# Kernel tuning notes

Measured on AMD Instinct MI355X. Metric: run time of the kernel, lower is better.

The kernel has to match this reference:

```python
import jax, jax.numpy as jnp
import numpy as np
import math

B, T, C, H = 2, 2048, 1024, 16


def setup_inputs() -> dict:
    key = jax.random.key(0)
    k1, k2, k3 = jax.random.split(key, 3)
    x = jax.random.normal(k1, (B, T, C), dtype=jnp.float32)
    qkv_w = jax.random.normal(k2, (3 * C, C), dtype=jnp.float32) * 0.02
    proj_w = jax.random.normal(k3, (C, C), dtype=jnp.float32) * 0.02
    distance_scales = jnp.full((H,), 0.1, dtype=jnp.float32)
    return {"x": x, "qkv_w": qkv_w, "proj_w": proj_w, "distance_scales": distance_scales}


def reference(x, qkv_w, proj_w, distance_scales):
    b, t, c = x.shape
    h = distance_scales.shape[0]
    dh = c // h
    scale = 1.0 / math.sqrt(dh)

    # torch Linear: y = x @ W^T ; split into q, k, v
    qkv = jnp.einsum('btc,oc->bto', x, qkv_w)  # [B,T,3C]
    q, k, v = jnp.split(qkv, 3, axis=-1)
    q = q.reshape(b, t, h, dh).transpose(0, 2, 1, 3)  # [B,H,T,Dh]
    k = k.reshape(b, t, h, dh).transpose(0, 2, 1, 3)
    v = v.reshape(b, t, h, dh).transpose(0, 2, 1, 3)

    logits = jnp.einsum('bhid,bhjd->bhij', q, k) * scale  # [B,H,T,T]

    idx = jnp.arange(t)
    dists = jnp.abs(idx[:, None] - idx[None, :]).astype(x.dtype)  # [T,T]
    logits = logits - distance_scales[None, :, None, None] * dists

    causal = idx[None, :] > idx[:, None]  # True above diagonal -> masked
    logits = jnp.where(causal[None, None, :, :], -jnp.inf, logits)

    attn = jax.nn.softmax(logits, axis=-1)  # [B,H,T,T]

    dist_energy = (attn * dists).sum(axis=-1).mean()
    flop_energy = -(attn * jnp.log(attn + 1e-9)).sum(axis=-1).mean()

    out = jnp.einsum('bhij,bhjd->bhid', attn, v)  # [B,H,T,Dh]
    out = out.transpose(0, 2, 1, 3).reshape(b, t, c)
    out = jnp.einsum('btc,oc->bto', out, proj_w)

    return (out, dist_energy, flop_energy, jax.lax.stop_gradient(attn), jax.lax.stop_gradient(dists))
```

## Files before the change

kernel.cpp:

```cpp
#include <hip/hip_runtime.h>
#include <hip/hip_bf16.h>
#include <math.h>

#define T_SEQ 2048
#define C3 3072
#define C_DIM 1024

typedef __bf16 bf16_t;
typedef __bf16 bf16x8 __attribute__((ext_vector_type(8)));
typedef __bf16 bf16x4_t __attribute__((ext_vector_type(4)));
typedef float f32x4 __attribute__((ext_vector_type(4)));

typedef __attribute__((address_space(1))) const void gconst_t;
typedef __attribute__((address_space(3))) void lds_t;

static __device__ __forceinline__ bf16x8 ldg8(const bf16_t* p) {
    return *reinterpret_cast<const bf16x8*>(p);
}

__global__ __launch_bounds__(256) void aux_kernel(const float* __restrict__ x,
                                                  const float* __restrict__ qw,
                                                  const float* __restrict__ pw,
                                                  bf16_t* __restrict__ xb,
                                                  bf16_t* __restrict__ wb,
                                                  bf16_t* __restrict__ pb,
                                                  float* __restrict__ dout,
                                                  float* __restrict__ ews) {
    long gid = (long)blockIdx.x * 256 + threadIdx.x;
    if (gid < 2) ews[gid] = 0.f;
    const float* src;
    bf16_t* dst;
    long u;
    if (gid < 1048576) { src = x; dst = xb; u = gid; }
    else if (gid < 1835008) { src = qw; dst = wb; u = gid - 1048576; }
    else if (gid < 2097152) { src = pw; dst = pb; u = gid - 1835008; }
    else {
        long v = gid - 2097152;
        long e0 = v << 2;
        int i = (int)(e0 >> 11), j0 = (int)(e0 & 2047);
        f32x4 o;
        for (int r = 0; r < 4; ++r) {
            int j = j0 + r;
            o[r] = (float)(i > j ? i - j : j - i);
        }
        __builtin_nontemporal_store(o, (f32x4*)(dout + e0));
        return;
    }
    float4 v4 = ((const float4*)src)[u];
    bf16x4_t o;
    o[0] = (bf16_t)v4.x; o[1] = (bf16_t)v4.y; o[2] = (bf16_t)v4.z; o[3] = (bf16_t)v4.w;
    *(bf16x4_t*)(dst + u * 4) = o;
}

template <int BM, bool OUT_BF16>
__global__ __launch_bounds__(256) void gemm_bt(const bf16_t* __restrict__ A,
                                               const bf16_t* __restrict__ Bw,
                                               void* __restrict__ Cout,
                                               int M, int N, int K) {
    constexpr int WM = BM / 2;
    constexpr int MI = WM / 16;
    __shared__ bf16_t sA[BM * 64];
    __shared__ bf16_t sB[128 * 64];
    int tid = threadIdx.x, lane = tid & 63, wid = tid >> 6;
    int m = lane & 15, quad = lane >> 4;
    int wm = (wid >> 1) * WM, wn = (wid & 1) * 64;
    int m0 = blockIdx.y * BM, n0 = blockIdx.x * 128;
    int lrow = lane >> 3, cxor = (lane & 7) ^ (lrow & 7);

    const bf16_t* Ag = A + (size_t)(m0 + wid * 8 + lrow) * K + cxor * 8;
    const bf16_t* Bg = Bw + (size_t)(n0 + wid * 8 + lrow) * K + cxor * 8;

    f32x4 acc[MI][4] = {};
    for (int k0 = 0; k0 < K; k0 += 64) {
        for (int p = 0; p < BM / 32; ++p)
            __builtin_amdgcn_global_load_lds((gconst_t*)(Ag + (size_t)(p * 32) * K + k0),
                                             (lds_t*)(sA + (p * 32 + wid * 8) * 64), 16, 0, 0);
        for (int p = 0; p < 4; ++p)
            __builtin_amdgcn_global_load_lds((gconst_t*)(Bg + (size_t)(p * 32) * K + k0),
                                             (lds_t*)(sB + (p * 32 + wid * 8) * 64), 16, 0, 0);
        __syncthreads();
        for (int ks = 0; ks < 2; ++ks) {
            bf16x8 a[MI], b[4];
            for (int i = 0; i < MI; ++i) {
                int r = wm + i * 16 + m;
                a[i] = *(const bf16x8*)(sA + r * 64 + ((((ks << 2) + quad) ^ (r & 7)) << 3));
            }
            for (int j = 0; j < 4; ++j) {
                int r = wn + j * 16 + m;
                b[j] = *(const bf16x8*)(sB + r * 64 + ((((ks << 2) + quad) ^ (r & 7)) << 3));
            }
            for (int i = 0; i < MI; ++i)
                for (int j = 0; j < 4; ++j)
                    acc[i][j] = __builtin_amdgcn_mfma_f32_16x16x32_bf16(b[j], a[i], acc[i][j], 0, 0, 0);
        }
        __syncthreads();
    }
    for (int i = 0; i < MI; ++i)
        for (int j = 0; j < 4; ++j) {
            size_t row = m0 + wm + i * 16 + m;
            int col = n0 + wn + j * 16 + quad * 4;
            if (OUT_BF16) {
                bf16x4_t o;
                for (int r = 0; r < 4; ++r) o[r] = (bf16_t)acc[i][j][r];
                *(bf16x4_t*)((bf16_t*)Cout + row * N + col) = o;
            } else {
                *(f32x4*)((float*)Cout + row * N + col) = acc[i][j];
            }
        }
}

__global__ __launch_bounds__(256) void repack_vt(const bf16_t* __restrict__ qkv,
                                                 bf16_t* __restrict__ vt) {
    __shared__ bf16_t s[64][72];
    int t0 = (blockIdx.x & 31) << 6;
    int bh = blockIdx.x >> 5;
    int b = bh >> 4, h = bh & 15;
    int tid = threadIdx.x;
    int r = tid >> 3, c8 = (tid & 7) << 3;
    const bf16_t* src = qkv + (size_t)(b * T_SEQ) * C3 + 2048 + h * 64;
    for (int p = 0; p < 2; ++p) {
        int t = r + p * 32;
        *(uint4*)&s[t][c8] = *(const uint4*)&src[(size_t)(t0 + t) * C3 + c8];
    }
    __syncthreads();
    bf16_t* dst = vt + (size_t)bh * 64 * T_SEQ;
    for (int p = 0; p < 2; ++p) {
        int d = r + p * 32;
        bf16x8 vv;
        for (int i = 0; i < 8; ++i) vv[i] = s[c8 + i][d];
        *(bf16x8*)&dst[(size_t)d * T_SEQ + t0 + c8] = vv;
    }
}

__global__ __launch_bounds__(256) void attn_kernel(const bf16_t* __restrict__ qkv,
                                                   const bf16_t* __restrict__ vt,
                                                   const float* __restrict__ dscales,
                                                   float* __restrict__ attn,
                                                   bf16_t* __restrict__ y,
                                                   float* __restrict__ ews) {
    __shared__ bf16_t sP[64][72];
    __shared__ float sred[8];
    int base = blockIdx.x & 31;
    int bh = blockIdx.x >> 5;
    int it = (bh & 8) ? (31 - base) : base;
    int b = bh >> 4, h = bh & 15;
    int i0 = it << 6;
    int tid = threadIdx.x, lane = tid & 63, wid = tid >> 6;
    int m = lane & 15, quad = lane >> 4;
    int w16 = wid << 4;
    float dsc = dscales[h];
    const float scale = 0.125f;

    int jskip = 0;
    if (dsc > 1e-6f) {
        int keep = (int)(38.0f / dsc + 63.0f) >> 6;
        jskip = it - keep;
        if (jskip < 0) jskip = 0;
    }

    const bf16_t* Qb = qkv + (size_t)(b * T_SEQ) * C3 + h * 64;
    const bf16_t* Kb = Qb + 1024;
    const bf16_t* Vb = vt + (size_t)bh * 64 * T_SEQ;
    float* Ab = attn + ((size_t)bh * T_SEQ + i0) * T_SEQ;

    int i = i0 + w16 + m;
    bf16x8 qf[2];
    qf[0] = ldg8(Qb + (size_t)i * C3 + quad * 8);
    qf[1] = ldg8(Qb + (size_t)i * C3 + 32 + quad * 8);

    float lsum = 0.f;
    for (int jt = jskip; jt <= it; ++jt) {
        int j0 = jt << 6;
        f32x4 acc[4] = {};
        for (int ks = 0; ks < 2; ++ks)
            for (int n = 0; n < 4; ++n) {
                bf16x8 kf = ldg8(Kb + (size_t)(j0 + n * 16 + m) * C3 + ks * 32 + quad * 8);
                acc[n] = __builtin_amdgcn_mfma_f32_16x16x32_bf16(kf, qf[ks], acc[n], 0, 0, 0);
            }
        if (jt < it) {
            for (int n = 0; n < 4; ++n)
                for (int r = 0; r < 4; ++r) {
                    float d = (float)(i - (j0 + n * 16 + quad * 4 + r));
                    lsum += __expf(acc[n][r] * scale - dsc * d);
                }
        } else {
            for (int n = 0; n < 4; ++n)
                for (int r = 0; r < 4; ++r) {
                    int j = j0 + n * 16 + quad * 4 + r;
                    if (j <= i) lsum += __expf(acc[n][r] * scale - dsc * (float)(i - j));
                }
        }
    }
    lsum += __shfl_xor(lsum, 16);
    lsum += __shfl_xor(lsum, 32);
    float rl = 1.f / lsum;

    f32x4 oacc[4] = {};
    float e_d = 0.f;
    float e_e = (quad == 0) ? -__logf(lsum) : 0.f;

    for (int jt = jskip; jt <= it; ++jt) {
        int j0 = jt << 6;
        f32x4 acc[4] = {};
        for (int ks = 0; ks < 2; ++ks)
            for (int n = 0; n < 4; ++n) {
                bf16x8 kf = ldg8(Kb + (size_t)(j0 + n * 16 + m) * C3 + ks * 32 + quad * 8);
                acc[n] = __builtin_amdgcn_mfma_f32_16x16x32_bf16(kf, qf[ks], acc[n], 0, 0, 0);
            }
        bool diag = (jt == it);
        for (int n = 0; n < 4; ++n) {
            f32x4 pv;
            for (int r = 0; r < 4; ++r) {
                int j = j0 + n * 16 + quad * 4 + r;
                float p = 0.f;
                if (!diag || j <= i) {
                    float d = (float)(i - j);
                    float v = acc[n][r] * scale - dsc * d;
                    p = __expf(v) * rl;
                    e_d += p * d;
                    e_e += p * v;
                }
                pv[r] = p;
            }
            __builtin_nontemporal_store(
                pv, (f32x4*)(Ab + (size_t)(w16 + m) * T_SEQ + j0 + n * 16 + quad * 4));
            bf16x4_t pb;
            for (int r = 0; r < 4; ++r) pb[r] = (bf16_t)pv[r];
            *(bf16x4_t*)&sP[w16 + m][n * 16 + quad * 4] = pb;
        }
        for (int ks = 0; ks < 2; ++ks) {
            bf16x8 pf = *(const bf16x8*)&sP[w16 + m][ks * 32 + quad * 8];
            for (int n = 0; n < 4; ++n) {
                bf16x8 vf = ldg8(Vb + (size_t)(n * 16 + m) * T_SEQ + j0 + ks * 32 + quad * 8);
                oacc[n] = __builtin_amdgcn_mfma_f32_16x16x32_bf16(vf, pf, oacc[n], 0, 0, 0);
            }
        }
    }

    for (int n = 0; n < 4; ++n) {
        bf16x4_t o;
        for (int r = 0; r < 4; ++r) o[r] = (bf16_t)oacc[n][r];
        *(bf16x4_t*)(y + (size_t)(b * T_SEQ + i) * C_DIM + h * 64 + n * 16 + quad * 4) = o;
    }

    for (int off = 1; off < 64; off <<= 1) {
        e_d += __shfl_xor(e_d, off);
        e_e += __shfl_xor(e_e, off);
    }
    if (lane == 0) { sred[wid] = e_d; sred[wid + 4] = e_e; }
    __syncthreads();
    if (tid == 0) {
        atomicAdd(ews, sred[0] + sred[1] + sred[2] + sred[3]);
        atomicAdd(ews + 1, sred[4] + sred[5] + sred[6] + sred[7]);
    }

    {
        f32x4 z4 = {0.f, 0.f, 0.f, 0.f};
        int ln = jskip << 6;
        for (int r = 0; r < 64; ++r) {
            float* rowp = Ab + (size_t)r * T_SEQ;
            for (int c = tid << 2; c < ln; c += 1024)
                __builtin_nontemporal_store(z4, (f32x4*)(rowp + c));
        }
        int zc0 = i0 + 64, zn = T_SEQ - zc0;
        for (int r = 0; r < 64; ++r) {
            float* rowp = Ab + (size_t)r * T_SEQ + zc0;
            for (int c = tid << 2; c < zn; c += 1024)
                __builtin_nontemporal_store(z4, (f32x4*)(rowp + c));
        }
    }
}

__global__ void finalize_kernel(const float* __restrict__ ews, float* __restrict__ dout) {
    dout[4194304] = ews[0] / 65536.f;
    dout[4194305] = -ews[1] / 65536.f;
}

extern "C" void kernel_launch(void* const* d_in, const int* in_sizes, int n_in,
                              void* d_out, int out_size, void* d_ws, size_t ws_size,
                              hipStream_t stream) {
    const float* x = (const float*)d_in[0];
    const float* qkv_w = (const float*)d_in[1];
    const float* proj_w = (const float*)d_in[2];
    const float* dscales = (const float*)d_in[3];
    float* out = (float*)d_out;

    char* ws = (char*)d_ws;
    float* ews   = (float*)ws;
    bf16_t* xb   = (bf16_t*)(ws + 256);
    bf16_t* wb   = xb + 4194304;
    bf16_t* pb   = wb + 3145728;
    bf16_t* qkvb = pb + 1048576;
    bf16_t* vtb  = qkvb + 12582912;
    bf16_t* yb   = vtb + 4194304;

    aux_kernel<<<12288, 256, 0, stream>>>(x, qkv_w, proj_w, xb, wb, pb,
                                          out + 138412034, ews);
    gemm_bt<128, true><<<dim3(24, 32), 256, 0, stream>>>(xb, wb, qkvb, 4096, 3072, 1024);
    repack_vt<<<1024, 256, 0, stream>>>(qkvb, vtb);
    attn_kernel<<<1024, 256, 0, stream>>>(qkvb, vtb, dscales, out + 4194306, yb, ews);
    gemm_bt<64, false><<<dim3(8, 64), 256, 0, stream>>>(yb, pb, out, 4096, 1024, 1024);
    finalize_kernel<<<1, 1, 0, stream>>>(ews, out);
}
```

Baseline: 864.3 us.

## Move attention zero-fill and dists writes into QKV GEMM extra blocks

The masked and skipped zero regions of the attention-probability output, and the full distance matrix, are now written by extra thread blocks appended to the QKV projection GEMM grid. Previously the zero-fill ran at the end of the attention kernel and the distances were written by the conversion kernel. The aim is to overlap these bandwidth-bound stores with the compute-bound GEMM and shorten the attention kernel's tail. The finalize kernel is folded into an extra block row of the output-projection GEMM, which removes one launch. The trade-off is that the store traffic now competes with the GEMM for memory bandwidth and the GEMM grid becomes larger and uneven.

```diff
diff --git a/kernel.cpp b/kernel.cpp
--- a/kernel.cpp
+++ b/kernel.cpp
@@ -24,7 +24,6 @@
                                                   bf16_t* __restrict__ xb,
                                                   bf16_t* __restrict__ wb,
                                                   bf16_t* __restrict__ pb,
-                                                  float* __restrict__ dout,
                                                   float* __restrict__ ews) {
     long gid = (long)blockIdx.x * 256 + threadIdx.x;
     if (gid < 2) ews[gid] = 0.f;
@@ -33,30 +32,76 @@
     long u;
     if (gid < 1048576) { src = x; dst = xb; u = gid; }
     else if (gid < 1835008) { src = qw; dst = wb; u = gid - 1048576; }
-    else if (gid < 2097152) { src = pw; dst = pb; u = gid - 1835008; }
-    else {
-        long v = gid - 2097152;
-        long e0 = v << 2;
-        int i = (int)(e0 >> 11), j0 = (int)(e0 & 2047);
-        f32x4 o;
-        for (int r = 0; r < 4; ++r) {
-            int j = j0 + r;
-            o[r] = (float)(i > j ? i - j : j - i);
-        }
-        __builtin_nontemporal_store(o, (f32x4*)(dout + e0));
-        return;
-    }
+    else { src = pw; dst = pb; u = gid - 1835008; }
     float4 v4 = ((const float4*)src)[u];
     bf16x4_t o;
     o[0] = (bf16_t)v4.x; o[1] = (bf16_t)v4.y; o[2] = (bf16_t)v4.z; o[3] = (bf16_t)v4.w;
     *(bf16x4_t*)(dst + u * 4) = o;
 }
 
-template <int BM, bool OUT_BF16>
+template <int BM, bool OUT_BF16, bool FUSE, bool FIN>
 __global__ __launch_bounds__(256) void gemm_bt(const bf16_t* __restrict__ A,
                                                const bf16_t* __restrict__ Bw,
                                                void* __restrict__ Cout,
-                                               int M, int N, int K) {
+                                               int M, int N, int K,
+                                               float* __restrict__ attn_zero,
+                                               const float* __restrict__ dscales,
+                                               float* __restrict__ dists,
+                                               const float* __restrict__ ews,
+                                               float* __restrict__ dout) {
+    if (FIN) {
+        if (blockIdx.y == gridDim.y - 1) {
+            if (blockIdx.x == 0 && threadIdx.x == 0) {
+                dout[4194304] = ews[0] / 65536.f;
+                dout[4194305] = -ews[1] / 65536.f;
+            }
+            return;
+        }
+    }
+    if (FUSE && blockIdx.y >= 32) {
+        int fb = (blockIdx.y - 32) * gridDim.x + blockIdx.x;
+        int tid = threadIdx.x;
+        f32x4 z4 = {0.f, 0.f, 0.f, 0.f};
+        if (fb < 1024) {
+            int bh = fb >> 5, it = fb & 31, h = bh & 15;
+            float dsc = dscales[h];
+            int jskip = 0;
+            if (dsc > 1e-6f) {
+                int keep = (int)(38.0f / dsc + 63.0f) >> 6;
+                jskip = it - keep;
+                if (jskip < 0) jskip = 0;
+            }
+            float* Ab = attn_zero + ((size_t)bh * T_SEQ + (it << 6)) * T_SEQ;
+            int ln = jskip << 6;
+            for (int r = 0; r < 64; ++r) {
+                float* rowp = Ab + (size_t)r * T_SEQ;
+                for (int c = tid << 2; c < ln; c += 1024)
+                    __builtin_nontemporal_store(z4, (f32x4*)(rowp + c));
+            }
+            int zc0 = (it << 6) + 64, zn = T_SEQ - zc0;
+            for (int r = 0; r < 64; ++r) {
+                float* rowp = Ab + (size_t)r * T_SEQ + zc0;
+                for (int c = tid << 2; c < zn; c += 1024)
+                    __builtin_nontemporal_store(z4, (f32x4*)(rowp + c));
+            }
+        } else {
+            int i0r = (fb - 1024) << 2;
+            for (int rr = 0; rr < 4; ++rr) {
+                int i = i0r + rr;
+                float* rowp = dists + (size_t)i * T_SEQ;
+                for (int c = tid << 2; c < T_SEQ; c += 1024) {
+                    f32x4 o;
+                    for (int k = 0; k < 4; ++k) {
+                        int j = c + k;
+                        o[k] = (float)(i > j ? i - j : j - i);
+                    }
+                    __builtin_nontemporal_store(o, (f32x4*)(rowp + c));
+                }
+            }
+        }
+        return;
+    }
+
     constexpr int WM = BM / 2;
     constexpr int MI = WM / 16;
     __shared__ bf16_t sA[BM * 64];
@@ -253,27 +298,6 @@
         atomicAdd(ews, sred[0] + sred[1] + sred[2] + sred[3]);
         atomicAdd(ews + 1, sred[4] + sred[5] + sred[6] + sred[7]);
     }
-
-    {
-        f32x4 z4 = {0.f, 0.f, 0.f, 0.f};
-        int ln = jskip << 6;
-        for (int r = 0; r < 64; ++r) {
-            float* rowp = Ab + (size_t)r * T_SEQ;
-            for (int c = tid << 2; c < ln; c += 1024)
-                __builtin_nontemporal_store(z4, (f32x4*)(rowp + c));
-        }
-        int zc0 = i0 + 64, zn = T_SEQ - zc0;
-        for (int r = 0; r < 64; ++r) {
-            float* rowp = Ab + (size_t)r * T_SEQ + zc0;
-            for (int c = tid << 2; c < zn; c += 1024)
-                __builtin_nontemporal_store(z4, (f32x4*)(rowp + c));
-        }
-    }
-}
-
-__global__ void finalize_kernel(const float* __restrict__ ews, float* __restrict__ dout) {
-    dout[4194304] = ews[0] / 65536.f;
-    dout[4194305] = -ews[1] / 65536.f;
 }
 
 extern "C" void kernel_launch(void* const* d_in, const int* in_sizes, int n_in,
@@ -294,11 +318,14 @@
     bf16_t* vtb  = qkvb + 12582912;
     bf16_t* yb   = vtb + 4194304;
 
-    aux_kernel<<<12288, 256, 0, stream>>>(x, qkv_w, proj_w, xb, wb, pb,
-                                          out + 138412034, ews);
-    gemm_bt<128, true><<<dim3(24, 32), 256, 0, stream>>>(xb, wb, qkvb, 4096, 3072, 1024);
+    float* attn_out = out + 4194306;
+    float* dists_out = out + 138412034;
+
+    aux_kernel<<<8192, 256, 0, stream>>>(x, qkv_w, proj_w, xb, wb, pb, ews);
+    gemm_bt<128, true, true, false><<<dim3(24, 96), 256, 0, stream>>>(
+        xb, wb, qkvb, 4096, 3072, 1024, attn_out, dscales, dists_out, nullptr, nullptr);
     repack_vt<<<1024, 256, 0, stream>>>(qkvb, vtb);
-    attn_kernel<<<1024, 256, 0, stream>>>(qkvb, vtb, dscales, out + 4194306, yb, ews);
-    gemm_bt<64, false><<<dim3(8, 64), 256, 0, stream>>>(yb, pb, out, 4096, 1024, 1024);
-    finalize_kernel<<<1, 1, 0, stream>>>(ews, out);
-}
+    attn_kernel<<<1024, 256, 0, stream>>>(qkvb, vtb, dscales, attn_out, yb, ews);
+    gemm_bt<64, false, false, true><<<dim3(8, 65), 256, 0, stream>>>(
+        yb, pb, out, 4096, 1024, 1024, nullptr, nullptr, nullptr, ews, out);
+}
```

Measured after the change: 885.5 us. 2.4% more time.
